# Kernel optimization log

Hardware: AMD Instinct MI355X
Metric: run time of the kernel (lower is better)

The kernel has to match this reference:

```python
import jax, jax.numpy as jnp
import numpy as np

N = 10000      # cells (nodes)
F_IN = 512     # genes (features)
H = 40         # hidden_dim
DEG = 16       # avg kNN degree
EPS = 1e-5     # GraphNorm eps


def gcn(x, W, b, src, dst, coef):
    # PyG GCNConv: transform then symmetric-normalized aggregate (+bias)
    h = x @ W                                   # [N, out]
    msg = h[src] * coef[:, None]                # [E, out]
    out = jax.ops.segment_sum(msg, dst, num_segments=N)
    return out + b


def graph_norm(x, weight, bias, alpha):
    # PyG GraphNorm over a single graph: mean/var across nodes, learnable mean scale
    mean = jnp.mean(x, axis=0, keepdims=True)
    shifted = x - alpha * mean
    var = jnp.mean(shifted * shifted, axis=0, keepdims=True)
    return weight * shifted * jax.lax.rsqrt(var + EPS) + bias


def setup_inputs() -> dict:
    key = jax.random.key(0)
    ks = jax.random.split(key, 8)
    x = jax.random.uniform(ks[0], (N, F_IN), dtype=jnp.float32)
    E = N * DEG
    src = jax.random.randint(ks[1], (E,), 0, N)
    dst = jax.random.randint(ks[2], (E,), 0, N)
    loop = jnp.arange(N)
    src = jnp.concatenate([src, loop])          # add self-loops (GCNConv default)
    dst = jnp.concatenate([dst, loop])

    def glorot(k, shape):
        lim = np.sqrt(6.0 / (shape[0] + shape[1])).astype(np.float32)
        return jax.random.uniform(k, shape, jnp.float32, -lim, lim)

    W1 = glorot(ks[3], (F_IN, H)); b1 = jnp.zeros((H,), jnp.float32)
    gn_w = jnp.ones((H,), jnp.float32)
    gn_b = jnp.zeros((H,), jnp.float32)
    gn_a = jnp.ones((H,), jnp.float32)          # mean_scale alpha
    Wm = glorot(ks[4], (H, F_IN)); bm = jnp.zeros((F_IN,), jnp.float32)
    Wd = glorot(ks[5], (H, F_IN)); bd = jnp.zeros((F_IN,), jnp.float32)
    Wp = glorot(ks[6], (H, F_IN)); bp = jnp.zeros((F_IN,), jnp.float32)
    return {"x": x, "src": src, "dst": dst, "W1": W1, "b1": b1,
            "gn_w": gn_w, "gn_b": gn_b, "gn_a": gn_a,
            "Wm": Wm, "bm": bm, "Wd": Wd, "bd": bd, "Wp": Wp, "bp": bp}


def reference(x, src, dst, W1, b1, gn_w, gn_b, gn_a, Wm, bm, Wd, bd, Wp, bp):
    # symmetric GCN normalization (self-loops already in edge list, so deg >= 1)
    deg = jax.ops.segment_sum(jnp.ones_like(src, dtype=x.dtype), dst, num_segments=N)
    dis = jax.lax.rsqrt(deg)
    coef = dis[src] * dis[dst]                  # [E]

    hidden = jax.nn.relu(graph_norm(gcn(x, W1, b1, src, dst, coef), gn_w, gn_b, gn_a))
    # Dropout(0.3) is identity at inference
    _mean = jnp.clip(jnp.exp(gcn(hidden, Wm, bm, src, dst, coef)), 1e-5, 1e6)
    _disp = jnp.clip(jax.nn.softplus(gcn(hidden, Wd, bd, src, dst, coef)), 1e-4, 1e4)
    _pi = jax.nn.sigmoid(gcn(hidden, Wp, bp, src, dst, coef))
    return (_mean, _disp, _pi)
```

## Files before the change

### kernel.cpp

```cpp
#include <hip/hip_runtime.h>
#include <math.h>

#define NN 10000
#define FIN 512
#define HD 40
#define GEPS 1e-5f

#define ZI4 ((2 * NN + 2 * HD) / 4)
#define MM1_BLOCKS ((NN + 15) / 16)
#define ZERO_BLOCKS ((ZI4 + 255) / 256)
#define CVT_BLOCKS ((3 * 32 * 3 * 64 + 255) / 256)

typedef _Float16 h4 __attribute__((ext_vector_type(4)));
typedef float f4 __attribute__((ext_vector_type(4)));

__global__ void k_hist(const int* __restrict__ dst, int* __restrict__ cnt, int E) {
    int e = blockIdx.x * blockDim.x + threadIdx.x;
    if (e < E) atomicAdd(&cnt[dst[e]], 1);
}

__global__ __launch_bounds__(1024) void k_scan(const int* __restrict__ cnt,
                                               int* __restrict__ rowstart,
                                               float* __restrict__ dis) {
    __shared__ int lds[1024];
    const int t = threadIdx.x;
    const int start = t * 16;
    int4 c[4];
    int s = 0;
    if (start < NN) {
#pragma unroll
        for (int q = 0; q < 4; ++q) {
            c[q] = *(const int4*)(cnt + start + q * 4);
            s += c[q].x + c[q].y + c[q].z + c[q].w;
        }
    }
    lds[t] = s;
    __syncthreads();
    for (int off = 1; off < 1024; off <<= 1) {
        int v = (t >= off) ? lds[t - off] : 0;
        __syncthreads();
        lds[t] += v;
        __syncthreads();
    }
    if (start < NN) {
        int run = lds[t] - s;
#pragma unroll
        for (int q = 0; q < 4; ++q) {
            int4 rs; float4 dv;
            rs.x = run; dv.x = rsqrtf((float)c[q].x); run += c[q].x;
            rs.y = run; dv.y = rsqrtf((float)c[q].y); run += c[q].y;
            rs.z = run; dv.z = rsqrtf((float)c[q].z); run += c[q].z;
            rs.w = run; dv.w = rsqrtf((float)c[q].w); run += c[q].w;
            *(int4*)(rowstart + start + q * 4) = rs;
            *(float4*)(dis + start + q * 4) = dv;
        }
        if (start + 16 == NN) rowstart[NN] = run;
    }
}

__global__ void k_fill(const int* __restrict__ src, const int* __restrict__ dst,
                       const int* __restrict__ rowstart, int* __restrict__ cur,
                       const float* __restrict__ dis, int2* __restrict__ csr, int E) {
    int e = blockIdx.x * blockDim.x + threadIdx.x;
    if (e >= E) return;
    int s = src[e], d = dst[e];
    int pos = rowstart[d] + atomicAdd(&cur[d], 1);
    int2 v;
    v.x = s;
    v.y = __float_as_int(dis[s] * dis[d]);
    csr[pos] = v;
}

__global__ __launch_bounds__(256) void k_mm1z(const float* __restrict__ x,
                                              const float* __restrict__ W1,
                                              float* __restrict__ h1,
                                              int4* __restrict__ zbuf,
                                              const float* __restrict__ Wm,
                                              const float* __restrict__ Wd,
                                              const float* __restrict__ Wp,
                                              _Float16* __restrict__ Whf) {
    if (blockIdx.x >= MM1_BLOCKS + ZERO_BLOCKS) {
        int idx = (blockIdx.x - MM1_BLOCKS - ZERO_BLOCKS) * 256 + threadIdx.x;
        if (idx < 3 * 32 * 3 * 64) {
            int lane = idx & 63;
            int kk   = (idx >> 6) % 3;
            int ct   = ((idx >> 6) / 3) % 32;
            int z    = idx / (64 * 3 * 32);
            const float* W = (z == 0) ? Wm : (z == 1) ? Wd : Wp;
            int col = ct * 16 + (lane & 15);
            h4 v;
#pragma unroll
            for (int j = 0; j < 4; ++j) {
                int krow = kk * 16 + (lane >> 4) * 4 + j;
                v[j] = (krow < HD) ? (_Float16)W[(size_t)krow * FIN + col] : (_Float16)0.f;
            }
            *(h4*)(Whf + (size_t)idx * 4) = v;
        }
        return;
    }
    if (blockIdx.x >= MM1_BLOCKS) {
        int i = (blockIdx.x - MM1_BLOCKS) * 256 + threadIdx.x;
        if (i < ZI4) zbuf[i] = make_int4(0, 0, 0, 0);
        return;
    }
    __shared__ float red[256 * 41];
    const int tid = threadIdx.x;
    const int r = tid & 15;
    const int kg = tid >> 4;
    const int row = blockIdx.x * 16 + r;
    const int rowc = min(row, NN - 1);
    const float4* xr = (const float4*)(x + (size_t)rowc * FIN + kg * 32);
    float acc[HD];
#pragma unroll
    for (int c = 0; c < HD; ++c) acc[c] = 0.f;
#pragma unroll 2
    for (int q = 0; q < 8; ++q) {
        float4 xv = xr[q];
        const float* wbase = W1 + (size_t)(kg * 32 + q * 4) * HD;
#pragma unroll
        for (int kk = 0; kk < 4; ++kk) {
            float xs = (kk == 0) ? xv.x : (kk == 1) ? xv.y : (kk == 2) ? xv.z : xv.w;
#pragma unroll
            for (int c4 = 0; c4 < 10; ++c4) {
                float4 wv = *(const float4*)(wbase + kk * HD + c4 * 4);
                acc[c4 * 4 + 0] = fmaf(xs, wv.x, acc[c4 * 4 + 0]);
                acc[c4 * 4 + 1] = fmaf(xs, wv.y, acc[c4 * 4 + 1]);
                acc[c4 * 4 + 2] = fmaf(xs, wv.z, acc[c4 * 4 + 2]);
                acc[c4 * 4 + 3] = fmaf(xs, wv.w, acc[c4 * 4 + 3]);
            }
        }
    }
#pragma unroll
    for (int c = 0; c < HD; ++c) red[tid * 41 + c] = acc[c];
    __syncthreads();
    if (tid < 160) {
        int rr = tid / 10, c4 = tid % 10;
        float o0 = 0.f, o1 = 0.f, o2 = 0.f, o3 = 0.f;
#pragma unroll
        for (int kg2 = 0; kg2 < 16; ++kg2) {
            const float* p = &red[(kg2 * 16 + rr) * 41 + c4 * 4];
            o0 += p[0]; o1 += p[1]; o2 += p[2]; o3 += p[3];
        }
        int orow = blockIdx.x * 16 + rr;
        if (orow < NN)
            *(float4*)&h1[(size_t)orow * HD + c4 * 4] = make_float4(o0, o1, o2, o3);
    }
}

__global__ __launch_bounds__(256) void k_gather1s(const int* __restrict__ rowstart,
                                                  const int2* __restrict__ csr,
                                                  const float* __restrict__ hin,
                                                  const float* __restrict__ b1,
                                                  float* __restrict__ agg1,
                                                  float* __restrict__ stats) {
    __shared__ float4 part[256];
    __shared__ float s0[HD], s1[HD];
    const int t = threadIdx.x;
    if (t < HD) { s0[t] = 0.f; s1[t] = 0.f; }
    __syncthreads();
    const int slot = blockIdx.x * 128 + (t & 127);
    const int half = t >> 7;
    float4 acc = make_float4(0.f, 0.f, 0.f, 0.f);
    if (slot < NN * 10) {
        const int n = slot / 10, c4 = slot % 10;
        const int j0 = rowstart[n], j1 = rowstart[n + 1];
        const int mid = j0 + ((j1 - j0 + 1) >> 1);
        const int ja = half ? mid : j0;
        const int jb = half ? j1 : mid;
        for (int j = ja; j < jb; j += 8) {
            const int jm = jb - 1;
            int2 e[8];
#pragma unroll
            for (int q = 0; q < 8; ++q) e[q] = csr[min(j + q, jm)];
            float4 v[8];
#pragma unroll
            for (int q = 0; q < 8; ++q)
                v[q] = *(const float4*)&hin[(size_t)e[q].x * HD + c4 * 4];
#pragma unroll
            for (int q = 0; q < 8; ++q) {
                float cf = (j + q < jb) ? __int_as_float(e[q].y) : 0.f;
                acc.x = fmaf(v[q].x, cf, acc.x);
                acc.y = fmaf(v[q].y, cf, acc.y);
                acc.z = fmaf(v[q].z, cf, acc.z);
                acc.w = fmaf(v[q].w, cf, acc.w);
            }
        }
    }
    part[t] = acc;
    __syncthreads();
    if (half == 0 && slot < NN * 10) {
        const int c4 = slot % 10;
        float4 p2 = part[t + 128];
        acc.x += p2.x; acc.y += p2.y; acc.z += p2.z; acc.w += p2.w;
        ((float4*)agg1)[slot] = acc;
        float4 bv = ((const float4*)b1)[c4];
        float vx = acc.x + bv.x, vy = acc.y + bv.y, vz = acc.z + bv.z, vw = acc.w + bv.w;
        atomicAdd(&s0[c4 * 4 + 0], vx); atomicAdd(&s0[c4 * 4 + 1], vy);
        atomicAdd(&s0[c4 * 4 + 2], vz); atomicAdd(&s0[c4 * 4 + 3], vw);
        atomicAdd(&s1[c4 * 4 + 0], vx * vx); atomicAdd(&s1[c4 * 4 + 1], vy * vy);
        atomicAdd(&s1[c4 * 4 + 2], vz * vz); atomicAdd(&s1[c4 * 4 + 3], vw * vw);
    }
    __syncthreads();
    if (t < HD) {
        atomicAdd(&stats[t], s0[t]);
        atomicAdd(&stats[HD + t], s1[t]);
    }
}

__device__ __forceinline__ float activate_rt(float z, int act) {
    if (act == 0) {
        return fminf(fmaxf(__expf(z), 1e-5f), 1e6f);
    } else if (act == 1) {
        float sp = fmaxf(z, 0.0f) + __logf(1.0f + __expf(-fabsf(z)));
        return fminf(fmaxf(sp, 1e-4f), 1e4f);
    }
    return __fdividef(1.0f, 1.0f + __expf(-z));
}

__global__ __launch_bounds__(512) void k_gheads(const int* __restrict__ rowstart,
                                                const int2* __restrict__ csr,
                                                const float* __restrict__ agg1,
                                                const float* __restrict__ stats,
                                                const float* __restrict__ b1,
                                                const float* __restrict__ gw,
                                                const float* __restrict__ gb,
                                                const float* __restrict__ ga,
                                                const _Float16* __restrict__ Whf,
                                                const float* __restrict__ bm,
                                                const float* __restrict__ bd,
                                                const float* __restrict__ bp,
                                                float* __restrict__ out) {
    __shared__ float csc[2 * HD];
    __shared__ float4 part[320];
    __shared__ _Float16 aggh_s[16 * 48];
    const int t = threadIdx.x;
    const int rowbase = blockIdx.x * 16;

    if (t < HD) {
        float m   = stats[t] * (1.0f / NN);
        float ex2 = stats[HD + t] * (1.0f / NN);
        float a   = ga[t];
        float var = ex2 - 2.0f * a * m * m + a * a * m * m;
        float sc  = gw[t] * rsqrtf(var + GEPS);
        csc[t]      = sc;
        csc[HD + t] = sc * (b1[t] - a * m) + gb[t];
    }
    __syncthreads();

    float4 acc = make_float4(0.f, 0.f, 0.f, 0.f);
    if (t < 320) {
        const int s = (t < 160) ? t : t - 160;
        const int half = (t < 160) ? 0 : 1;
        const int row = s / 10, c4 = s % 10;
        const int n = rowbase + row;
        const int j0 = rowstart[n], j1 = rowstart[n + 1];
        const int mid = j0 + ((j1 - j0 + 1) >> 1);
        const int ja = half ? mid : j0;
        const int jb = half ? j1 : mid;
        float4 sc = ((const float4*)csc)[c4];
        float4 sh = ((const float4*)csc)[10 + c4];
        for (int j = ja; j < jb; j += 8) {
            const int jm = jb - 1;
            int2 e[8];
#pragma unroll
            for (int q = 0; q < 8; ++q) e[q] = csr[min(j + q, jm)];
            float4 v[8];
#pragma unroll
            for (int q = 0; q < 8; ++q)
                v[q] = *(const float4*)&agg1[(size_t)e[q].x * HD + c4 * 4];
#pragma unroll
            for (int q = 0; q < 8; ++q) {
                float cf = (j + q < jb) ? __int_as_float(e[q].y) : 0.f;
                v[q].x = fmaxf(fmaf(sc.x, v[q].x, sh.x), 0.f);
                v[q].y = fmaxf(fmaf(sc.y, v[q].y, sh.y), 0.f);
                v[q].z = fmaxf(fmaf(sc.z, v[q].z, sh.z), 0.f);
                v[q].w = fmaxf(fmaf(sc.w, v[q].w, sh.w), 0.f);
                acc.x = fmaf(v[q].x, cf, acc.x);
                acc.y = fmaf(v[q].y, cf, acc.y);
                acc.z = fmaf(v[q].z, cf, acc.z);
                acc.w = fmaf(v[q].w, cf, acc.w);
            }
        }
        part[t] = acc;
    }
    __syncthreads();
    if (t < 160) {
        const int row = t / 10, c4 = t % 10;
        float4 p2 = part[t + 160];
        acc.x += p2.x; acc.y += p2.y; acc.z += p2.z; acc.w += p2.w;
        h4 hv = { (_Float16)acc.x, (_Float16)acc.y, (_Float16)acc.z, (_Float16)acc.w };
        *(h4*)(aggh_s + row * 48 + c4 * 4) = hv;
        if (c4 == 0) {
            h4 zv = { (_Float16)0.f, (_Float16)0.f, (_Float16)0.f, (_Float16)0.f };
            *(h4*)(aggh_s + row * 48 + 40) = zv;
            *(h4*)(aggh_s + row * 48 + 44) = zv;
        }
    }
    __syncthreads();

    const int lane = t & 63;
    const int wvi  = t >> 6;
    const int r16  = lane & 15;
    const int kgrp = lane >> 4;
    const _Float16* arow = aggh_s + r16 * 48 + kgrp * 4;
    h4 g0 = *(const h4*)(arow);
    h4 g1 = *(const h4*)(arow + 16);
    h4 g2 = *(const h4*)(arow + 32);
    const int grow = rowbase + r16;

#pragma unroll
    for (int i = 0; i < 12; ++i) {
        const int job = wvi * 12 + i;
        const int z = job >> 5;
        const int ct = job & 31;
        const float* bias = (z == 0) ? bm : (z == 1) ? bd : bp;
        const _Float16* wb = Whf + ((size_t)(z * 32 + ct) * 3) * 256 + lane * 4;
        h4 w0 = *(const h4*)(wb);
        h4 w1 = *(const h4*)(wb + 256);
        h4 w2 = *(const h4*)(wb + 512);
        f4 a = {0.f, 0.f, 0.f, 0.f};
        a = __builtin_amdgcn_mfma_f32_16x16x16f16(w0, g0, a, 0, 0, 0);
        a = __builtin_amdgcn_mfma_f32_16x16x16f16(w1, g1, a, 0, 0, 0);
        a = __builtin_amdgcn_mfma_f32_16x16x16f16(w2, g2, a, 0, 0, 0);
        const int col0 = ct * 16 + kgrp * 4;
        float4 bv = *(const float4*)&bias[col0];
        float4 ov;
        ov.x = activate_rt(a[0] + bv.x, z);
        ov.y = activate_rt(a[1] + bv.y, z);
        ov.z = activate_rt(a[2] + bv.z, z);
        ov.w = activate_rt(a[3] + bv.w, z);
        *(float4*)(out + (size_t)z * NN * FIN + (size_t)grow * FIN + col0) = ov;
    }
}

extern "C" void kernel_launch(void* const* d_in, const int* in_sizes, int n_in,
                              void* d_out, int out_size, void* d_ws, size_t ws_size,
                              hipStream_t stream) {
    const float* x   = (const float*)d_in[0];
    const int*   src = (const int*)d_in[1];
    const int*   dst = (const int*)d_in[2];
    const float* W1  = (const float*)d_in[3];
    const float* b1  = (const float*)d_in[4];
    const float* gnw = (const float*)d_in[5];
    const float* gnb = (const float*)d_in[6];
    const float* gna = (const float*)d_in[7];
    const float* Wm  = (const float*)d_in[8];
    const float* bm  = (const float*)d_in[9];
    const float* Wd  = (const float*)d_in[10];
    const float* bd  = (const float*)d_in[11];
    const float* Wp  = (const float*)d_in[12];
    const float* bp  = (const float*)d_in[13];
    const int E = in_sizes[1];

    float*     ws       = (float*)d_ws;
    float*     h1       = ws;
    float*     agg1     = h1 + (size_t)NN * HD;
    int*       cnt      = (int*)(agg1 + (size_t)NN * HD);
    int*       cur      = cnt + NN;
    float*     stats    = (float*)(cur + NN);
    float*     dis      = stats + 2 * HD;
    int*       rowstart = (int*)(dis + NN);
    int2*      csr      = (int2*)(rowstart + NN + 2);
    _Float16*  Whf      = (_Float16*)(csr + E);
    float*     out      = (float*)d_out;

    k_mm1z<<<MM1_BLOCKS + ZERO_BLOCKS + CVT_BLOCKS, 256, 0, stream>>>(
        x, W1, h1, (int4*)cnt, Wm, Wd, Wp, Whf);
    k_hist<<<(E + 255) / 256, 256, 0, stream>>>(dst, cnt, E);
    k_scan<<<1, 1024, 0, stream>>>(cnt, rowstart, dis);
    k_fill<<<(E + 255) / 256, 256, 0, stream>>>(src, dst, rowstart, cur, dis, csr, E);
    const int gblocks = (NN * 10 + 127) / 128;
    k_gather1s<<<gblocks, 256, 0, stream>>>(rowstart, csr, h1, b1, agg1, stats);
    k_gheads<<<MM1_BLOCKS, 512, 0, stream>>>(rowstart, csr, agg1, stats,
                                             b1, gnw, gnb, gna,
                                             Whf, bm, bd, bp, out);
}
```

Baseline: 125.5 us.

## Split gather and head GEMM kernels; fuse histogram with first matmul

The fused gather-plus-heads kernel is split in two. A standalone gather kernel writes the normalized aggregate as fp16 into the workspace, reusing the h1 buffer. A separate MFMA heads kernel then runs one grid z-slice per output head with 256-thread blocks, which gives more parallelism in the write-heavy output stage. Separately, the edge histogram is merged into the first matmul launch and zeroing/weight conversion moves to its own small kernel, so the histogram overlaps with the matmul. The split adds one launch and a round-trip of the aggregate through global memory.

```diff
diff --git a/kernel.cpp b/kernel.cpp
--- a/kernel.cpp
+++ b/kernel.cpp
@@ -14,9 +14,86 @@
 typedef _Float16 h4 __attribute__((ext_vector_type(4)));
 typedef float f4 __attribute__((ext_vector_type(4)));
 
-__global__ void k_hist(const int* __restrict__ dst, int* __restrict__ cnt, int E) {
-    int e = blockIdx.x * blockDim.x + threadIdx.x;
-    if (e < E) atomicAdd(&cnt[dst[e]], 1);
+__global__ __launch_bounds__(256) void k_zc(int4* __restrict__ zbuf,
+                                            const float* __restrict__ Wm,
+                                            const float* __restrict__ Wd,
+                                            const float* __restrict__ Wp,
+                                            _Float16* __restrict__ Whf) {
+    if (blockIdx.x < ZERO_BLOCKS) {
+        int i = blockIdx.x * 256 + threadIdx.x;
+        if (i < ZI4) zbuf[i] = make_int4(0, 0, 0, 0);
+        return;
+    }
+    int idx = (blockIdx.x - ZERO_BLOCKS) * 256 + threadIdx.x;
+    if (idx < 3 * 32 * 3 * 64) {
+        int lane = idx & 63;
+        int kk   = (idx >> 6) % 3;
+        int ct   = ((idx >> 6) / 3) % 32;
+        int z    = idx / (64 * 3 * 32);
+        const float* W = (z == 0) ? Wm : (z == 1) ? Wd : Wp;
+        int col = ct * 16 + (lane & 15);
+        h4 v;
+#pragma unroll
+        for (int j = 0; j < 4; ++j) {
+            int krow = kk * 16 + (lane >> 4) * 4 + j;
+            v[j] = (krow < HD) ? (_Float16)W[(size_t)krow * FIN + col] : (_Float16)0.f;
+        }
+        *(h4*)(Whf + (size_t)idx * 4) = v;
+    }
+}
+
+__global__ __launch_bounds__(256) void k_histmm1(const float* __restrict__ x,
+                                                 const float* __restrict__ W1,
+                                                 float* __restrict__ h1,
+                                                 const int* __restrict__ dst,
+                                                 int* __restrict__ cnt, int E) {
+    if (blockIdx.x >= MM1_BLOCKS) {
+        int e = (blockIdx.x - MM1_BLOCKS) * 256 + threadIdx.x;
+        if (e < E) atomicAdd(&cnt[dst[e]], 1);
+        return;
+    }
+    __shared__ float red[256 * 41];
+    const int tid = threadIdx.x;
+    const int r = tid & 15;
+    const int kg = tid >> 4;
+    const int row = blockIdx.x * 16 + r;
+    const int rowc = min(row, NN - 1);
+    const float4* xr = (const float4*)(x + (size_t)rowc * FIN + kg * 32);
+    float acc[HD];
+#pragma unroll
+    for (int c = 0; c < HD; ++c) acc[c] = 0.f;
+#pragma unroll 2
+    for (int q = 0; q < 8; ++q) {
+        float4 xv = xr[q];
+        const float* wbase = W1 + (size_t)(kg * 32 + q * 4) * HD;
+#pragma unroll
+        for (int kk = 0; kk < 4; ++kk) {
+            float xs = (kk == 0) ? xv.x : (kk == 1) ? xv.y : (kk == 2) ? xv.z : xv.w;
+#pragma unroll
+            for (int c4 = 0; c4 < 10; ++c4) {
+                float4 wv = *(const float4*)(wbase + kk * HD + c4 * 4);
+                acc[c4 * 4 + 0] = fmaf(xs, wv.x, acc[c4 * 4 + 0]);
+                acc[c4 * 4 + 1] = fmaf(xs, wv.y, acc[c4 * 4 + 1]);
+                acc[c4 * 4 + 2] = fmaf(xs, wv.z, acc[c4 * 4 + 2]);
+                acc[c4 * 4 + 3] = fmaf(xs, wv.w, acc[c4 * 4 + 3]);
+            }
+        }
+    }
+#pragma unroll
+    for (int c = 0; c < HD; ++c) red[tid * 41 + c] = acc[c];
+    __syncthreads();
+    if (tid < 160) {
+        int rr = tid / 10, c4 = tid % 10;
+        float o0 = 0.f, o1 = 0.f, o2 = 0.f, o3 = 0.f;
+#pragma unroll
+        for (int kg2 = 0; kg2 < 16; ++kg2) {
+            const float* p = &red[(kg2 * 16 + rr) * 41 + c4 * 4];
+            o0 += p[0]; o1 += p[1]; o2 += p[2]; o3 += p[3];
+        }
+        int orow = blockIdx.x * 16 + rr;
+        if (orow < NN)
+            *(float4*)&h1[(size_t)orow * HD + c4 * 4] = make_float4(o0, o1, o2, o3);
+    }
 }
 
 __global__ __launch_bounds__(1024) void k_scan(const int* __restrict__ cnt,
@@ -69,82 +146,6 @@
     v.x = s;
     v.y = __float_as_int(dis[s] * dis[d]);
     csr[pos] = v;
-}
-
-__global__ __launch_bounds__(256) void k_mm1z(const float* __restrict__ x,
-                                              const float* __restrict__ W1,
-                                              float* __restrict__ h1,
-                                              int4* __restrict__ zbuf,
-                                              const float* __restrict__ Wm,
-                                              const float* __restrict__ Wd,
-                                              const float* __restrict__ Wp,
-                                              _Float16* __restrict__ Whf) {
-    if (blockIdx.x >= MM1_BLOCKS + ZERO_BLOCKS) {
-        int idx = (blockIdx.x - MM1_BLOCKS - ZERO_BLOCKS) * 256 + threadIdx.x;
-        if (idx < 3 * 32 * 3 * 64) {
-            int lane = idx & 63;
-            int kk   = (idx >> 6) % 3;
-            int ct   = ((idx >> 6) / 3) % 32;
-            int z    = idx / (64 * 3 * 32);
-            const float* W = (z == 0) ? Wm : (z == 1) ? Wd : Wp;
-            int col = ct * 16 + (lane & 15);
-            h4 v;
-#pragma unroll
-            for (int j = 0; j < 4; ++j) {
-                int krow = kk * 16 + (lane >> 4) * 4 + j;
-                v[j] = (krow < HD) ? (_Float16)W[(size_t)krow * FIN + col] : (_Float16)0.f;
-            }
-            *(h4*)(Whf + (size_t)idx * 4) = v;
-        }
-        return;
-    }
-    if (blockIdx.x >= MM1_BLOCKS) {
-        int i = (blockIdx.x - MM1_BLOCKS) * 256 + threadIdx.x;
-        if (i < ZI4) zbuf[i] = make_int4(0, 0, 0, 0);
-        return;
-    }
-    __shared__ float red[256 * 41];
-    const int tid = threadIdx.x;
-    const int r = tid & 15;
-    const int kg = tid >> 4;
-    const int row = blockIdx.x * 16 + r;
-    const int rowc = min(row, NN - 1);
-    const float4* xr = (const float4*)(x + (size_t)rowc * FIN + kg * 32);
-    float acc[HD];
-#pragma unroll
-    for (int c = 0; c < HD; ++c) acc[c] = 0.f;
-#pragma unroll 2
-    for (int q = 0; q < 8; ++q) {
-        float4 xv = xr[q];
-        const float* wbase = W1 + (size_t)(kg * 32 + q * 4) * HD;
-#pragma unroll
-        for (int kk = 0; kk < 4; ++kk) {
-            float xs = (kk == 0) ? xv.x : (kk == 1) ? xv.y : (kk == 2) ? xv.z : xv.w;
-#pragma unroll
-            for (int c4 = 0; c4 < 10; ++c4) {
-                float4 wv = *(const float4*)(wbase + kk * HD + c4 * 4);
-                acc[c4 * 4 + 0] = fmaf(xs, wv.x, acc[c4 * 4 + 0]);
-                acc[c4 * 4 + 1] = fmaf(xs, wv.y, acc[c4 * 4 + 1]);
-                acc[c4 * 4 + 2] = fmaf(xs, wv.z, acc[c4 * 4 + 2]);
-                acc[c4 * 4 + 3] = fmaf(xs, wv.w, acc[c4 * 4 + 3]);
-            }
-        }
-    }
-#pragma unroll
-    for (int c = 0; c < HD; ++c) red[tid * 41 + c] = acc[c];
-    __syncthreads();
-    if (tid < 160) {
-        int rr = tid / 10, c4 = tid % 10;
-        float o0 = 0.f, o1 = 0.f, o2 = 0.f, o3 = 0.f;
-#pragma unroll
-        for (int kg2 = 0; kg2 < 16; ++kg2) {
-            const float* p = &red[(kg2 * 16 + rr) * 41 + c4 * 4];
-            o0 += p[0]; o1 += p[1]; o2 += p[2]; o3 += p[3];
-        }
-        int orow = blockIdx.x * 16 + rr;
-        if (orow < NN)
-            *(float4*)&h1[(size_t)orow * HD + c4 * 4] = make_float4(o0, o1, o2, o3);
-    }
 }
 
 __global__ __launch_bounds__(256) void k_gather1s(const int* __restrict__ rowstart,
@@ -207,35 +208,18 @@
     }
 }
 
-__device__ __forceinline__ float activate_rt(float z, int act) {
-    if (act == 0) {
-        return fminf(fmaxf(__expf(z), 1e-5f), 1e6f);
-    } else if (act == 1) {
-        float sp = fmaxf(z, 0.0f) + __logf(1.0f + __expf(-fabsf(z)));
-        return fminf(fmaxf(sp, 1e-4f), 1e4f);
-    }
-    return __fdividef(1.0f, 1.0f + __expf(-z));
-}
-
-__global__ __launch_bounds__(512) void k_gheads(const int* __restrict__ rowstart,
-                                                const int2* __restrict__ csr,
-                                                const float* __restrict__ agg1,
-                                                const float* __restrict__ stats,
-                                                const float* __restrict__ b1,
-                                                const float* __restrict__ gw,
-                                                const float* __restrict__ gb,
-                                                const float* __restrict__ ga,
-                                                const _Float16* __restrict__ Whf,
-                                                const float* __restrict__ bm,
-                                                const float* __restrict__ bd,
-                                                const float* __restrict__ bp,
-                                                float* __restrict__ out) {
+__global__ __launch_bounds__(256) void k_gather2(const int* __restrict__ rowstart,
+                                                 const int2* __restrict__ csr,
+                                                 const float* __restrict__ agg1,
+                                                 const float* __restrict__ stats,
+                                                 const float* __restrict__ b1,
+                                                 const float* __restrict__ gw,
+                                                 const float* __restrict__ gb,
+                                                 const float* __restrict__ ga,
+                                                 _Float16* __restrict__ aggout_h) {
+    __shared__ float4 part[256];
     __shared__ float csc[2 * HD];
-    __shared__ float4 part[320];
-    __shared__ _Float16 aggh_s[16 * 48];
     const int t = threadIdx.x;
-    const int rowbase = blockIdx.x * 16;
-
     if (t < HD) {
         float m   = stats[t] * (1.0f / NN);
         float ex2 = stats[HD + t] * (1.0f / NN);
@@ -246,13 +230,11 @@
         csc[HD + t] = sc * (b1[t] - a * m) + gb[t];
     }
     __syncthreads();
-
+    const int slot = blockIdx.x * 128 + (t & 127);
+    const int half = t >> 7;
     float4 acc = make_float4(0.f, 0.f, 0.f, 0.f);
-    if (t < 320) {
-        const int s = (t < 160) ? t : t - 160;
-        const int half = (t < 160) ? 0 : 1;
-        const int row = s / 10, c4 = s % 10;
-        const int n = rowbase + row;
+    if (slot < NN * 10) {
+        const int n = slot / 10, c4 = slot % 10;
         const int j0 = rowstart[n], j1 = rowstart[n + 1];
         const int mid = j0 + ((j1 - j0 + 1) >> 1);
         const int ja = half ? mid : j0;
@@ -281,55 +263,76 @@
                 acc.w = fmaf(v[q].w, cf, acc.w);
             }
         }
-        part[t] = acc;
-    }
-    __syncthreads();
-    if (t < 160) {
-        const int row = t / 10, c4 = t % 10;
-        float4 p2 = part[t + 160];
+    }
+    part[t] = acc;
+    __syncthreads();
+    if (half == 0 && slot < NN * 10) {
+        const int n = slot / 10, c4 = slot % 10;
+        float4 p2 = part[t + 128];
         acc.x += p2.x; acc.y += p2.y; acc.z += p2.z; acc.w += p2.w;
         h4 hv = { (_Float16)acc.x, (_Float16)acc.y, (_Float16)acc.z, (_Float16)acc.w };
-        *(h4*)(aggh_s + row * 48 + c4 * 4) = hv;
+        *(h4*)(aggout_h + (size_t)n * 48 + c4 * 4) = hv;
         if (c4 == 0) {
             h4 zv = { (_Float16)0.f, (_Float16)0.f, (_Float16)0.f, (_Float16)0.f };
-            *(h4*)(aggh_s + row * 48 + 40) = zv;
-            *(h4*)(aggh_s + row * 48 + 44) = zv;
-        }
-    }
-    __syncthreads();
-
-    const int lane = t & 63;
-    const int wvi  = t >> 6;
+            *(h4*)(aggout_h + (size_t)n * 48 + 40) = zv;
+            *(h4*)(aggout_h + (size_t)n * 48 + 44) = zv;
+        }
+    }
+}
+
+__device__ __forceinline__ float activate_rt(float z, int act) {
+    if (act == 0) {
+        return fminf(fmaxf(__expf(z), 1e-5f), 1e6f);
+    } else if (act == 1) {
+        float sp = fmaxf(z, 0.0f) + __logf(1.0f + __expf(-fabsf(z)));
+        return fminf(fmaxf(sp, 1e-4f), 1e4f);
+    }
+    return __fdividef(1.0f, 1.0f + __expf(-z));
+}
+
+__global__ __launch_bounds__(256) void k_heads3m(const _Float16* __restrict__ agghh,
+                                                 const _Float16* __restrict__ Whf,
+                                                 const float* __restrict__ bm,
+                                                 const float* __restrict__ bd,
+                                                 const float* __restrict__ bp,
+                                                 float* __restrict__ out) {
+    const int z = blockIdx.z;
+    const float* bias = (z == 0) ? bm : (z == 1) ? bd : bp;
+    float* o = out + (size_t)z * NN * FIN;
+
+    const int lane = threadIdx.x & 63;
+    const int wv   = threadIdx.x >> 6;
+    const int rowbase = blockIdx.x * 16;
     const int r16  = lane & 15;
     const int kgrp = lane >> 4;
-    const _Float16* arow = aggh_s + r16 * 48 + kgrp * 4;
+
+    const _Float16* arow = agghh + (size_t)(rowbase + r16) * 48 + kgrp * 4;
     h4 g0 = *(const h4*)(arow);
     h4 g1 = *(const h4*)(arow + 16);
     h4 g2 = *(const h4*)(arow + 32);
+
     const int grow = rowbase + r16;
-
-#pragma unroll
-    for (int i = 0; i < 12; ++i) {
-        const int job = wvi * 12 + i;
-        const int z = job >> 5;
-        const int ct = job & 31;
-        const float* bias = (z == 0) ? bm : (z == 1) ? bd : bp;
+    float* orow = o + (size_t)grow * FIN;
+
+#pragma unroll
+    for (int i = 0; i < 8; ++i) {
+        const int ct = wv * 8 + i;
         const _Float16* wb = Whf + ((size_t)(z * 32 + ct) * 3) * 256 + lane * 4;
         h4 w0 = *(const h4*)(wb);
         h4 w1 = *(const h4*)(wb + 256);
         h4 w2 = *(const h4*)(wb + 512);
-        f4 a = {0.f, 0.f, 0.f, 0.f};
-        a = __builtin_amdgcn_mfma_f32_16x16x16f16(w0, g0, a, 0, 0, 0);
-        a = __builtin_amdgcn_mfma_f32_16x16x16f16(w1, g1, a, 0, 0, 0);
-        a = __builtin_amdgcn_mfma_f32_16x16x16f16(w2, g2, a, 0, 0, 0);
+        f4 acc = {0.f, 0.f, 0.f, 0.f};
+        acc = __builtin_amdgcn_mfma_f32_16x16x16f16(w0, g0, acc, 0, 0, 0);
+        acc = __builtin_amdgcn_mfma_f32_16x16x16f16(w1, g1, acc, 0, 0, 0);
+        acc = __builtin_amdgcn_mfma_f32_16x16x16f16(w2, g2, acc, 0, 0, 0);
         const int col0 = ct * 16 + kgrp * 4;
         float4 bv = *(const float4*)&bias[col0];
         float4 ov;
-        ov.x = activate_rt(a[0] + bv.x, z);
-        ov.y = activate_rt(a[1] + bv.y, z);
-        ov.z = activate_rt(a[2] + bv.z, z);
-        ov.w = activate_rt(a[3] + bv.w, z);
-        *(float4*)(out + (size_t)z * NN * FIN + (size_t)grow * FIN + col0) = ov;
+        ov.x = activate_rt(acc[0] + bv.x, z);
+        ov.y = activate_rt(acc[1] + bv.y, z);
+        ov.z = activate_rt(acc[2] + bv.z, z);
+        ov.w = activate_rt(acc[3] + bv.w, z);
+        *(float4*)(orow + col0) = ov;
     }
 }
 
@@ -362,16 +365,18 @@
     int*       rowstart = (int*)(dis + NN);
     int2*      csr      = (int2*)(rowstart + NN + 2);
     _Float16*  Whf      = (_Float16*)(csr + E);
+    _Float16*  agghh    = (_Float16*)h1;
     float*     out      = (float*)d_out;
 
-    k_mm1z<<<MM1_BLOCKS + ZERO_BLOCKS + CVT_BLOCKS, 256, 0, stream>>>(
-        x, W1, h1, (int4*)cnt, Wm, Wd, Wp, Whf);
-    k_hist<<<(E + 255) / 256, 256, 0, stream>>>(dst, cnt, E);
+    k_zc<<<ZERO_BLOCKS + CVT_BLOCKS, 256, 0, stream>>>((int4*)cnt, Wm, Wd, Wp, Whf);
+    const int histb = (E + 255) / 256;
+    k_histmm1<<<MM1_BLOCKS + histb, 256, 0, stream>>>(x, W1, h1, dst, cnt, E);
     k_scan<<<1, 1024, 0, stream>>>(cnt, rowstart, dis);
     k_fill<<<(E + 255) / 256, 256, 0, stream>>>(src, dst, rowstart, cur, dis, csr, E);
     const int gblocks = (NN * 10 + 127) / 128;
     k_gather1s<<<gblocks, 256, 0, stream>>>(rowstart, csr, h1, b1, agg1, stats);
-    k_gheads<<<MM1_BLOCKS, 512, 0, stream>>>(rowstart, csr, agg1, stats,
-                                             b1, gnw, gnb, gna,
-                                             Whf, bm, bd, bp, out);
-}
+    k_gather2<<<gblocks, 256, 0, stream>>>(rowstart, csr, agg1, stats,
+                                           b1, gnw, gnb, gna, agghh);
+    dim3 hgrid(MM1_BLOCKS, 1, 3);
+    k_heads3m<<<hgrid, 256, 0, stream>>>(agghh, Whf, bm, bd, bp, out);
+}
```

Measured after the change: 119.9 us. 1.05x faster.
